# Kernel tuning notes

Hardware: AMD Instinct MI355X
Metric: run time of the kernel (lower is better)

The kernel has to match this reference:

```python
import jax, jax.numpy as jnp
import numpy as np

EPS = 1e-5

def _act_quant(x, bits=8):
    # per-token absmax quantization to signed int range, dequantized (STE)
    qb = float(2 ** (bits - 1) - 1)  # 127 for 8 bits
    scale = qb / jnp.clip(jnp.max(jnp.abs(x), axis=-1, keepdims=True), EPS, None)
    x_dq = jnp.clip(jnp.round(x * scale), -qb, qb) / scale
    return x + jax.lax.stop_gradient(x_dq - x)

def _weight_quant(w):
    # BitNet b1.58 ternary weights: scale = mean |W|, values in {-1,0,1} * scale (STE)
    s = jnp.clip(jnp.mean(jnp.abs(w)), EPS, None)
    w_dq = jnp.clip(jnp.round(w / s), -1.0, 1.0) * s
    return w + jax.lax.stop_gradient(w_dq - w)

def _bitlinear(x, w, bits=8):
    # x: [..., in], w: [out, in]
    return jnp.einsum('bsi,oi->bso', _act_quant(x, bits), _weight_quant(w))

def setup_inputs() -> dict:
    key = jax.random.key(0)
    k1, k2, k3 = jax.random.split(key, 3)
    B, S, H = 4, 4096, 2048
    I = int(H * 2.0)
    return {
        'hidden_states': jax.random.normal(k1, (B, S, H), dtype=jnp.float32),
        'w_up': jax.random.normal(k2, (I, H), dtype=jnp.float32) * (1.0 / np.sqrt(H)),
        'w_down': jax.random.normal(k3, (H, I), dtype=jnp.float32) * (1.0 / np.sqrt(I)),
    }

def reference(hidden_states, w_up, w_down):
    bits = 8
    h = _bitlinear(hidden_states, w_up, bits)          # [B,S,I]
    h = jnp.square(jax.nn.relu(h))                      # squared ReLU
    # dropout p=0.0 (eval) -> identity
    out = _bitlinear(h, w_down, bits)                   # [B,S,H]
    return out
```

## Files before the change

kernel.cpp:

```cpp
#include <hip/hip_runtime.h>
#include <hip/hip_bf16.h>

typedef signed char i8_t;
typedef _Float16 half_t;
typedef float v4fl __attribute__((ext_vector_type(4)));
typedef _Float16 v8h __attribute__((ext_vector_type(8)));
typedef int v4i __attribute__((ext_vector_type(4)));
typedef signed char v8c __attribute__((ext_vector_type(8)));
typedef signed char v16c __attribute__((ext_vector_type(16)));

__device__ __forceinline__ float ternqf(float w, float s) {
    float q = rintf(w / s);
    return fminf(1.f, fmaxf(-1.f, q));
}

__device__ __forceinline__ void gload16(const void* g, void* l) {
    __builtin_amdgcn_global_load_lds(
        (const __attribute__((address_space(1))) void*)g,
        (__attribute__((address_space(3))) void*)l, 16, 0, 0);
}

__global__ void abssum_partial(const float* __restrict__ w, long n,
                               float* __restrict__ partial) {
    long i0 = ((long)blockIdx.x * 256 + threadIdx.x) * 8;
    long stride = (long)gridDim.x * 256 * 8;
    float s = 0.f;
    for (long i = i0; i < n; i += stride) {
        v4fl a = *(const v4fl*)(w + i);
        v4fl b = *(const v4fl*)(w + i + 4);
#pragma unroll
        for (int j = 0; j < 4; ++j) s += fabsf(a[j]) + fabsf(b[j]);
    }
#pragma unroll
    for (int off = 32; off > 0; off >>= 1) s += __shfl_down(s, off, 64);
    __shared__ __align__(16) float red[4];
    if ((threadIdx.x & 63) == 0) red[threadIdx.x >> 6] = s;
    __syncthreads();
    if (threadIdx.x == 0)
        partial[blockIdx.x] = (red[0] + red[1]) + (red[2] + red[3]);
}

__global__ void abssum_final(const float* __restrict__ part_up,
                             const float* __restrict__ part_dn,
                             float* __restrict__ scales, float inv) {
    const int wv = threadIdx.x >> 6;
    const int l = threadIdx.x & 63;
    const float* part = wv ? part_dn : part_up;
    float s = ((part[l] + part[l + 64]) + (part[l + 128] + part[l + 192]));
#pragma unroll
    for (int off = 32; off > 0; off >>= 1) s += __shfl_down(s, off, 64);
    if (l == 0) scales[wv] = fmaxf(s * inv, 1e-5f);
}

__global__ void wquant_kernel(const float* __restrict__ w, i8_t* __restrict__ wq,
                              const float* __restrict__ scale) {
    float s = scale[0];
    long i = ((long)blockIdx.x * 256 + threadIdx.x) * 8;
    v4fl a = *(const v4fl*)(w + i);
    v4fl b = *(const v4fl*)(w + i + 4);
    v8c o;
#pragma unroll
    for (int j = 0; j < 4; ++j) {
        o[j]     = (i8_t)(int)ternqf(a[j], s);
        o[j + 4] = (i8_t)(int)ternqf(b[j], s);
    }
    *(v8c*)(wq + i) = o;
}

template <int W>
__global__ void rowquant_kernel(const float* __restrict__ src, i8_t* __restrict__ dst,
                                float* __restrict__ scale_out, int rows) {
    const int l = threadIdx.x & 63;
    const int row = blockIdx.x * 4 + (threadIdx.x >> 6);
    if (row >= rows) return;
    const int NI = W / 1024;
    const float* p = src + (size_t)row * W + l * 16;
    float v[NI * 16];
#pragma unroll
    for (int it = 0; it < NI; ++it) {
#pragma unroll
        for (int c = 0; c < 4; ++c) {
            v4fl a = *(const v4fl*)(p + it * 1024 + c * 4);
#pragma unroll
            for (int e = 0; e < 4; ++e) v[it * 16 + c * 4 + e] = a[e];
        }
    }
    float amax = 0.f;
#pragma unroll
    for (int j = 0; j < NI * 16; ++j) amax = fmaxf(amax, fabsf(v[j]));
#pragma unroll
    for (int off = 32; off > 0; off >>= 1)
        amax = fmaxf(amax, __shfl_xor(amax, off, 64));
    const float m = fmaxf(amax, 1e-5f);
    if (l == 0) scale_out[row] = m / 127.f;
    const float sc = 127.f / m;
    i8_t* q = dst + (size_t)row * W + l * 16;
#pragma unroll
    for (int it = 0; it < NI; ++it) {
        v16c o;
#pragma unroll
        for (int j = 0; j < 16; ++j) {
            float t = rintf(v[it * 16 + j] * sc);
            o[j] = (i8_t)(int)fminf(127.f, fmaxf(-127.f, t));
        }
        *(v16c*)(q + it * 1024) = o;
    }
}

template <typename T, int NV>
__global__ void hamax_kernel(const T* __restrict__ h, float* __restrict__ scale_out,
                             float* __restrict__ recip_out) {
    const int row = blockIdx.x;
    const int tid = threadIdx.x;
    const T* p = h + (size_t)row * (NV * 2048);
    float amax = 0.f;
#pragma unroll
    for (int it = 0; it < NV; ++it) {
        const T* s = p + ((size_t)it * 256 + tid) * 8;
#pragma unroll
        for (int j = 0; j < 8; ++j) amax = fmaxf(amax, fabsf((float)s[j]));
    }
#pragma unroll
    for (int off = 32; off > 0; off >>= 1) amax = fmaxf(amax, __shfl_xor(amax, off, 64));
    __shared__ __align__(16) float red[4];
    if ((tid & 63) == 0) red[tid >> 6] = amax;
    __syncthreads();
    if (tid == 0) {
        float m = fmaxf(fmaxf(red[0], red[1]), fmaxf(red[2], red[3]));
        m = fmaxf(m, 1e-5f);
        scale_out[row] = m / 127.f;
        recip_out[row] = 127.f / m;
    }
}

__device__ __forceinline__ void stage_tile256(const i8_t* __restrict__ g, int K,
                                              i8_t* l, int tid) {
#pragma unroll
    for (int i = 0; i < 4; ++i) {
        const int c = i * 512 + tid;
        const int r = c >> 3;
        const int lc = (((c & 7) ^ (r & 7)) << 4);
        gload16(g + (size_t)r * K + lc, l + c * 16);
    }
}

#define MIDBAR() do { \
    __builtin_amdgcn_s_barrier(); \
    __builtin_amdgcn_sched_barrier(0); \
    asm volatile("s_waitcnt lgkmcnt(0)" ::: "memory"); \
    __builtin_amdgcn_sched_barrier(0); } while (0)

#define ENDBAR() do { \
    __builtin_amdgcn_sched_barrier(0); \
    __builtin_amdgcn_s_barrier(); \
    __builtin_amdgcn_sched_barrier(0); } while (0)

template <int EPI>
__launch_bounds__(512, 2)
__global__ void gemm_bt8(const i8_t* __restrict__ A, const i8_t* __restrict__ B,
                         void* __restrict__ Cv,
                         const float* __restrict__ rowscale,
                         const float* __restrict__ wscale,
                         int M, int N, int K) {
    __shared__ __align__(16) i8_t smem[131072];

    const int tid = threadIdx.x;

    const int gx = gridDim.x;
    const int nwg = gx * gridDim.y;
    int flat = blockIdx.y * gx + blockIdx.x;
    if ((nwg & 7) == 0) flat = (flat & 7) * (nwg >> 3) + (flat >> 3);
    const int n0 = (flat % gx) * 256;
    const int m0 = (flat / gx) * 256;

    const i8_t* gA = A + (size_t)m0 * K;
    const i8_t* gB = B + (size_t)n0 * K;

    const int w = tid >> 6, l = tid & 63;
    const int wr = w >> 2, wc = w & 3;
    const int lrow = l & 15, lq = l >> 4;
    const int lr7 = lrow & 7;
    const int kk0 = ((lq)     ^ lr7) << 4;
    const int kk1 = ((lq + 4) ^ lr7) << 4;
    const int aBase = ((wr * 128 + lrow) << 7);
    const int bBase = ((wc * 64 + lrow) << 7);

    v4i acc[8][4];
#pragma unroll
    for (int a = 0; a < 8; ++a)
#pragma unroll
        for (int b = 0; b < 4; ++b) acc[a][b] = (v4i){0, 0, 0, 0};

    const int NT = K >> 7;
    stage_tile256(gB, K, smem + 32768, tid);
    stage_tile256(gA, K, smem, tid);
    stage_tile256(gB + 128, K, smem + 65536 + 32768, tid);
    stage_tile256(gA + 128, K, smem + 65536, tid);
    asm volatile("s_waitcnt vmcnt(8)" ::: "memory");
    __builtin_amdgcn_s_barrier();
    __builtin_amdgcn_sched_barrier(0);

    for (int t = 0; t < NT; ++t) {
        i8_t* Ab = smem + ((t & 1) << 16);
        i8_t* Bb = Ab + 32768;
        const bool pf = (t + 2 < NT);

        v4i a0[4], a1[4], b0[4], b1[4];

#pragma unroll
        for (int mi = 0; mi < 4; ++mi)
            a0[mi] = *(const v4i*)(Ab + aBase + (mi << 11) + kk0);
#pragma unroll
        for (int nj = 0; nj < 4; ++nj)
            b0[nj] = *(const v4i*)(Bb + bBase + (nj << 11) + kk0);
        MIDBAR();
        __builtin_amdgcn_s_setprio(1);
#pragma unroll
        for (int mi = 0; mi < 4; ++mi)
#pragma unroll
            for (int nj = 0; nj < 4; ++nj)
                acc[mi][nj] = __builtin_amdgcn_mfma_i32_16x16x64_i8(
                    a0[mi], b0[nj], acc[mi][nj], 0, 0, 0);
        __builtin_amdgcn_s_setprio(0);
        ENDBAR();

#pragma unroll
        for (int mi = 0; mi < 4; ++mi)
            a1[mi] = *(const v4i*)(Ab + aBase + ((mi + 4) << 11) + kk0);
#pragma unroll
        for (int nj = 0; nj < 4; ++nj)
            b1[nj] = *(const v4i*)(Bb + bBase + (nj << 11) + kk1);
        MIDBAR();
        __builtin_amdgcn_s_setprio(1);
#pragma unroll
        for (int mi = 0; mi < 4; ++mi)
#pragma unroll
            for (int nj = 0; nj < 4; ++nj)
                acc[mi + 4][nj] = __builtin_amdgcn_mfma_i32_16x16x64_i8(
                    a1[mi], b0[nj], acc[mi + 4][nj], 0, 0, 0);
        __builtin_amdgcn_s_setprio(0);
        ENDBAR();

#pragma unroll
        for (int mi = 0; mi < 4; ++mi)
            a0[mi] = *(const v4i*)(Ab + aBase + (mi << 11) + kk1);
#pragma unroll
        for (int mi = 0; mi < 4; ++mi)
            a1[mi] = *(const v4i*)(Ab + aBase + ((mi + 4) << 11) + kk1);
        MIDBAR();
        __builtin_amdgcn_s_setprio(1);
#pragma unroll
        for (int mi = 0; mi < 4; ++mi)
#pragma unroll
            for (int nj = 0; nj < 4; ++nj)
                acc[mi][nj] = __builtin_amdgcn_mfma_i32_16x16x64_i8(
                    a0[mi], b1[nj], acc[mi][nj], 0, 0, 0);
        __builtin_amdgcn_s_setprio(0);
        ENDBAR();

        if (pf) {
            stage_tile256(gB + (size_t)(t + 2) * 128, K, Bb, tid);
            stage_tile256(gA + (size_t)(t + 2) * 128, K, Ab, tid);
        }
        MIDBAR();
        __builtin_amdgcn_s_setprio(1);
#pragma unroll
        for (int mi = 0; mi < 4; ++mi)
#pragma unroll
            for (int nj = 0; nj < 4; ++nj)
                acc[mi + 4][nj] = __builtin_amdgcn_mfma_i32_16x16x64_i8(
                    a1[mi], b1[nj], acc[mi + 4][nj], 0, 0, 0);
        __builtin_amdgcn_s_setprio(0);
        __builtin_amdgcn_sched_barrier(0);
        if (pf) {
            asm volatile("s_waitcnt vmcnt(8)" ::: "memory");
        } else if (t + 1 < NT) {
            asm volatile("s_waitcnt vmcnt(0)" ::: "memory");
        }
        if (t + 1 < NT) {
            __builtin_amdgcn_s_barrier();
            __builtin_amdgcn_sched_barrier(0);
        }
    }

    const float sw = wscale[0];
#pragma unroll
    for (int mi = 0; mi < 8; ++mi) {
#pragma unroll
        for (int r = 0; r < 4; ++r) {
            const int row = m0 + wr * 128 + mi * 16 + lq * 4 + r;
            const float rs = sw * rowscale[row];
#pragma unroll
            for (int nj = 0; nj < 4; ++nj) {
                const int col = n0 + wc * 64 + nj * 16 + lrow;
                float v = (float)acc[mi][nj][r] * rs;
                if (EPI == 0) {
                    ((float*)Cv)[(size_t)row * N + col] = v;
                } else {
                    v = fmaxf(v, 0.f); v = v * v;
                    ((float*)Cv)[(size_t)row * N + col] = v;
                }
            }
        }
    }
}

template <int ASRC, int EPI>
__launch_bounds__(256, 2)
__global__ void gemm_bt(const void* __restrict__ Av, const i8_t* __restrict__ B,
                        void* __restrict__ Cv,
                        const float* __restrict__ rowscale,
                        const float* __restrict__ arecip,
                        const float* __restrict__ wscale,
                        int M, int N, int K) {
    __shared__ __align__(16) i8_t As[128 * 64];
    __shared__ __align__(16) i8_t Bs[128 * 64];

    const int tid = threadIdx.x;
    const int gx = gridDim.x;
    const int nwg = gx * gridDim.y;
    int flat = blockIdx.y * gx + blockIdx.x;
    if ((nwg & 7) == 0) flat = (flat & 7) * (nwg >> 3) + (flat >> 3);
    const int n0 = (flat % gx) * 128;
    const int m0 = (flat / gx) * 128;

    const int srow = tid >> 2;
    const int scol = (tid & 3) * 16;
    const i8_t* gB0 = B + (size_t)(n0 + srow) * K + scol;
    const i8_t* gB1 = B + (size_t)(n0 + 64 + srow) * K + scol;
    i8_t* lB0 = Bs + tid * 16;
    i8_t* lB1 = Bs + 4096 + tid * 16;

    const i8_t* gA0 = nullptr;
    const i8_t* gA1 = nullptr;
    i8_t* lA0 = As + tid * 16;
    i8_t* lA1 = As + 4096 + tid * 16;
    if (ASRC == 0) {
        gA0 = (const i8_t*)Av + (size_t)(m0 + srow) * K + scol;
        gA1 = (const i8_t*)Av + (size_t)(m0 + 64 + srow) * K + scol;
    }

    const int qrow = tid >> 1;
    const int qcol = (tid & 1) * 32;
    const float* gA32 = (const float*)Av + (size_t)(m0 + qrow) * K + qcol;
    const half_t* gAh = (const half_t*)Av + (size_t)(m0 + qrow) * K + qcol;
    i8_t* qdst = As + qrow * 64 + qcol;
    const float qsc = (ASRC != 0) ? arecip[m0 + qrow] : 0.f;

    const int w = tid >> 6, l = tid & 63;
    const int wr = w >> 1, wc = w & 1;
    const int lrow = l & 15, lq = l >> 4;

    v4i acc[4][4];
#pragma unroll
    for (int a = 0; a < 4; ++a)
#pragma unroll
        for (int b = 0; b < 4; ++b) acc[a][b] = (v4i){0, 0, 0, 0};

    const int kiters = K / 64;
    for (int kt = 0; kt < kiters; ++kt) {
        const int off = kt * 64;
        v16c r0, r1;
        if (ASRC == 1) {
#pragma unroll
            for (int c = 0; c < 4; ++c) {
                v4fl f0 = *(const v4fl*)(gA32 + off + c * 4);
                v4fl f1 = *(const v4fl*)(gA32 + off + 16 + c * 4);
#pragma unroll
                for (int e = 0; e < 4; ++e) {
                    float t0 = rintf(f0[e] * qsc);
                    float t1 = rintf(f1[e] * qsc);
                    r0[c * 4 + e] = (i8_t)(int)fminf(127.f, fmaxf(-127.f, t0));
                    r1[c * 4 + e] = (i8_t)(int)fminf(127.f, fmaxf(-127.f, t1));
                }
            }
        } else if (ASRC == 2) {
#pragma unroll
            for (int c = 0; c < 2; ++c) {
                v8h h0 = *(const v8h*)(gAh + off + c * 8);
                v8h h1 = *(const v8h*)(gAh + off + 16 + c * 8);
#pragma unroll
                for (int e = 0; e < 8; ++e) {
                    float t0 = rintf((float)h0[e] * qsc);
                    float t1 = rintf((float)h1[e] * qsc);
                    r0[c * 8 + e] = (i8_t)(int)fminf(127.f, fmaxf(-127.f, t0));
                    r1[c * 8 + e] = (i8_t)(int)fminf(127.f, fmaxf(-127.f, t1));
                }
            }
        }
        __syncthreads();
        gload16(gB0 + off, lB0);
        gload16(gB1 + off, lB1);
        if (ASRC == 0) {
            gload16(gA0 + off, lA0);
            gload16(gA1 + off, lA1);
        } else {
            *(v16c*)qdst = r0;
            *(v16c*)(qdst + 16) = r1;
        }
        __syncthreads();

        v4i af[4], bfr[4];
#pragma unroll
        for (int mi = 0; mi < 4; ++mi)
            af[mi] = *(const v4i*)(As + (wr * 64 + mi * 16 + lrow) * 64 + lq * 16);
#pragma unroll
        for (int nj = 0; nj < 4; ++nj)
            bfr[nj] = *(const v4i*)(Bs + (wc * 64 + nj * 16 + lrow) * 64 + lq * 16);
#pragma unroll
        for (int mi = 0; mi < 4; ++mi)
#pragma unroll
            for (int nj = 0; nj < 4; ++nj)
                acc[mi][nj] = __builtin_amdgcn_mfma_i32_16x16x64_i8(
                    af[mi], bfr[nj], acc[mi][nj], 0, 0, 0);
    }

    const float sw = wscale[0];
#pragma unroll
    for (int mi = 0; mi < 4; ++mi) {
#pragma unroll
        for (int r = 0; r < 4; ++r) {
            const int row = m0 + wr * 64 + mi * 16 + lq * 4 + r;
            const float rs = sw * rowscale[row];
#pragma unroll
            for (int nj = 0; nj < 4; ++nj) {
                const int col = n0 + wc * 64 + nj * 16 + lrow;
                float v = (float)acc[mi][nj][r] * rs;
                if (EPI == 0) {
                    ((float*)Cv)[(size_t)row * N + col] = v;
                } else if (EPI == 1) {
                    v = fmaxf(v, 0.f); v = v * v;
                    ((half_t*)Cv)[(size_t)row * N + col] = (half_t)v;
                } else {
                    v = fmaxf(v, 0.f); v = v * v;
                    ((float*)Cv)[(size_t)row * N + col] = v;
                }
            }
        }
    }
}

extern "C" void kernel_launch(void* const* d_in, const int* in_sizes, int n_in,
                              void* d_out, int out_size, void* d_ws, size_t ws_size,
                              hipStream_t stream) {
    const float* x   = (const float*)d_in[0];
    const float* wup = (const float*)d_in[1];
    const float* wdn = (const float*)d_in[2];

    const int H = 2048;
    const int T = in_sizes[0] / H;
    const int I = in_sizes[1] / H;
    const long nw = (long)in_sizes[1];
    const float winv = 1.0f / (float)nw;

    char* p = (char*)d_ws;
    float* scales  = (float*)p;
    float* part_up = (float*)(p + 256);
    float* part_dn = (float*)(p + 1280);
    float* a_scale = (float*)(p + 2304);
    float* h_scale = a_scale + T;
    float* h_recip = h_scale + T;
    size_t off = 2304 + (size_t)12 * T;
    off = (off + 255) & ~(size_t)255;
    i8_t* xq  = (i8_t*)(p + off); off += (size_t)T * H;
    off = (off + 255) & ~(size_t)255;
    i8_t* wqu = (i8_t*)(p + off); off += (size_t)I * H;
    off = (off + 255) & ~(size_t)255;
    i8_t* wqd = (i8_t*)(p + off); off += (size_t)H * I;
    off = (off + 255) & ~(size_t)255;
    void* h  = (void*)(p + off);
    i8_t* hq = (i8_t*)(p + off + (size_t)T * I * 4);

    const size_t need_full = off + (size_t)T * I * 5;
    const size_t need_h32  = off + (size_t)T * I * 4;
    const int mode = (ws_size == 0 || need_full <= ws_size) ? 0
                   : (need_h32 <= ws_size ? 1 : 2);
    const bool big_ok = (T % 256 == 0) && (I % 256 == 0) && (H % 256 == 0) &&
                        (H >= 256) && (I >= 256);

    abssum_partial<<<256, 256, 0, stream>>>(wup, nw, part_up);
    abssum_partial<<<256, 256, 0, stream>>>(wdn, nw, part_dn);
    abssum_final<<<1, 128, 0, stream>>>(part_up, part_dn, scales, winv);

    int wblocks = (int)(nw / 2048);
    wquant_kernel<<<wblocks, 256, 0, stream>>>(wup, wqu, scales + 0);
    wquant_kernel<<<wblocks, 256, 0, stream>>>(wdn, wqd, scales + 1);

    rowquant_kernel<2048><<<(T + 3) / 4, 256, 0, stream>>>(x, xq, a_scale, T);

    if (mode == 0 && big_ok) {
        gemm_bt8<2><<<dim3(I / 256, T / 256), 512, 0, stream>>>(
            xq, wqu, h, a_scale, scales + 0, T, I, H);
        rowquant_kernel<4096><<<(T + 3) / 4, 256, 0, stream>>>(
            (const float*)h, hq, h_scale, T);
        gemm_bt8<0><<<dim3(H / 256, T / 256), 512, 0, stream>>>(
            hq, wqd, d_out, h_scale, scales + 1, T, H, I);
    } else if (mode == 0) {
        gemm_bt<0, 2><<<dim3(I / 128, T / 128), 256, 0, stream>>>(
            xq, wqu, h, a_scale, nullptr, scales + 0, T, I, H);
        rowquant_kernel<4096><<<(T + 3) / 4, 256, 0, stream>>>(
            (const float*)h, hq, h_scale, T);
        gemm_bt<0, 0><<<dim3(H / 128, T / 128), 256, 0, stream>>>(
            hq, wqd, d_out, h_scale, nullptr, scales + 1, T, H, I);
    } else if (mode == 1) {
        gemm_bt<0, 2><<<dim3(I / 128, T / 128), 256, 0, stream>>>(
            xq, wqu, h, a_scale, nullptr, scales + 0, T, I, H);
        hamax_kernel<float, 2><<<T, 256, 0, stream>>>((const float*)h, h_scale, h_recip);
        gemm_bt<1, 0><<<dim3(H / 128, T / 128), 256, 0, stream>>>(
            h, wqd, d_out, h_scale, h_recip, scales + 1, T, H, I);
    } else {
        gemm_bt<0, 1><<<dim3(I / 128, T / 128), 256, 0, stream>>>(
            xq, wqu, h, a_scale, nullptr, scales + 0, T, I, H);
        hamax_kernel<half_t, 2><<<T, 256, 0, stream>>>((const half_t*)h, h_scale, h_recip);
        gemm_bt<2, 0><<<dim3(H / 128, T / 128), 256, 0, stream>>>(
            h, wqd, d_out, h_scale, h_recip, scales + 1, T, H, I);
    }
}
```

Before: 652.8 us.

## Load B operand directly from global into registers, halve LDS, fewer barriers

The int8 GEMM no longer stages the B (weight) tile through LDS. Each wave loads its B fragments straight from global memory into registers, prefetching the next K-tile into a second register set. Only A is double-buffered in LDS, so LDS use halves and the per-iteration barriers drop from several to two. The cost is more VGPR pressure from the register prefetch buffers, and B loads are now redundant across the wave rows (two waves load the same B) with less coalesced access, which may add global traffic or stalls.

```diff
diff --git a/kernel.cpp b/kernel.cpp
--- a/kernel.cpp
+++ b/kernel.cpp
@@ -144,17 +144,6 @@
     }
 }
 
-#define MIDBAR() do { \
-    __builtin_amdgcn_s_barrier(); \
-    __builtin_amdgcn_sched_barrier(0); \
-    asm volatile("s_waitcnt lgkmcnt(0)" ::: "memory"); \
-    __builtin_amdgcn_sched_barrier(0); } while (0)
-
-#define ENDBAR() do { \
-    __builtin_amdgcn_sched_barrier(0); \
-    __builtin_amdgcn_s_barrier(); \
-    __builtin_amdgcn_sched_barrier(0); } while (0)
-
 template <int EPI>
 __launch_bounds__(512, 2)
 __global__ void gemm_bt8(const i8_t* __restrict__ A, const i8_t* __restrict__ B,
@@ -162,7 +151,7 @@
                          const float* __restrict__ rowscale,
                          const float* __restrict__ wscale,
                          int M, int N, int K) {
-    __shared__ __align__(16) i8_t smem[131072];
+    __shared__ __align__(16) i8_t Asm[65536];
 
     const int tid = threadIdx.x;
 
@@ -174,7 +163,6 @@
     const int m0 = (flat / gx) * 256;
 
     const i8_t* gA = A + (size_t)m0 * K;
-    const i8_t* gB = B + (size_t)n0 * K;
 
     const int w = tid >> 6, l = tid & 63;
     const int wr = w >> 2, wc = w & 3;
@@ -183,7 +171,8 @@
     const int kk0 = ((lq)     ^ lr7) << 4;
     const int kk1 = ((lq + 4) ^ lr7) << 4;
     const int aBase = ((wr * 128 + lrow) << 7);
-    const int bBase = ((wc * 64 + lrow) << 7);
+
+    const i8_t* gBl = B + (size_t)(n0 + wc * 64 + lrow) * K + lq * 16;
 
     v4i acc[8][4];
 #pragma unroll
@@ -191,93 +180,88 @@
 #pragma unroll
         for (int b = 0; b < 4; ++b) acc[a][b] = (v4i){0, 0, 0, 0};
 
+    v4i bcur[4][2], bnxt[4][2];
+
     const int NT = K >> 7;
-    stage_tile256(gB, K, smem + 32768, tid);
-    stage_tile256(gA, K, smem, tid);
-    stage_tile256(gB + 128, K, smem + 65536 + 32768, tid);
-    stage_tile256(gA + 128, K, smem + 65536, tid);
-    asm volatile("s_waitcnt vmcnt(8)" ::: "memory");
+    stage_tile256(gA, K, Asm, tid);
+#pragma unroll
+    for (int nj = 0; nj < 4; ++nj)
+#pragma unroll
+        for (int ks = 0; ks < 2; ++ks)
+            bcur[nj][ks] = *(const v4i*)(gBl + (size_t)(nj * 16) * K + ks * 64);
+    stage_tile256(gA + 128, K, Asm + 32768, tid);
+    asm volatile("s_waitcnt vmcnt(4)" ::: "memory");
     __builtin_amdgcn_s_barrier();
     __builtin_amdgcn_sched_barrier(0);
 
     for (int t = 0; t < NT; ++t) {
-        i8_t* Ab = smem + ((t & 1) << 16);
-        i8_t* Bb = Ab + 32768;
-        const bool pf = (t + 2 < NT);
-
-        v4i a0[4], a1[4], b0[4], b1[4];
-
-#pragma unroll
-        for (int mi = 0; mi < 4; ++mi)
+        i8_t* Ab = Asm + ((t & 1) << 15);
+        const bool pf1 = (t + 1 < NT);
+        const bool pf2 = (t + 2 < NT);
+
+        v4i a0[8], a1[8];
+
+#pragma unroll
+        for (int mi = 0; mi < 8; ++mi)
             a0[mi] = *(const v4i*)(Ab + aBase + (mi << 11) + kk0);
-#pragma unroll
-        for (int nj = 0; nj < 4; ++nj)
-            b0[nj] = *(const v4i*)(Bb + bBase + (nj << 11) + kk0);
-        MIDBAR();
+        if (pf1) {
+            const size_t koff = (size_t)(t + 1) * 128;
+#pragma unroll
+            for (int nj = 0; nj < 4; ++nj)
+#pragma unroll
+                for (int ks = 0; ks < 2; ++ks)
+                    bnxt[nj][ks] = *(const v4i*)(gBl + (size_t)(nj * 16) * K + koff + ks * 64);
+        }
+        __builtin_amdgcn_sched_barrier(0);
         __builtin_amdgcn_s_setprio(1);
 #pragma unroll
-        for (int mi = 0; mi < 4; ++mi)
+        for (int mi = 0; mi < 8; ++mi)
 #pragma unroll
             for (int nj = 0; nj < 4; ++nj)
                 acc[mi][nj] = __builtin_amdgcn_mfma_i32_16x16x64_i8(
-                    a0[mi], b0[nj], acc[mi][nj], 0, 0, 0);
+                    a0[mi], bcur[nj][0], acc[mi][nj], 0, 0, 0);
         __builtin_amdgcn_s_setprio(0);
-        ENDBAR();
-
+
+#pragma unroll
+        for (int mi = 0; mi < 8; ++mi)
+            a1[mi] = *(const v4i*)(Ab + aBase + (mi << 11) + kk1);
+        __builtin_amdgcn_sched_barrier(0);
+        __builtin_amdgcn_s_setprio(1);
 #pragma unroll
         for (int mi = 0; mi < 4; ++mi)
-            a1[mi] = *(const v4i*)(Ab + aBase + ((mi + 4) << 11) + kk0);
-#pragma unroll
-        for (int nj = 0; nj < 4; ++nj)
-            b1[nj] = *(const v4i*)(Bb + bBase + (nj << 11) + kk1);
-        MIDBAR();
+#pragma unroll
+            for (int nj = 0; nj < 4; ++nj)
+                acc[mi][nj] = __builtin_amdgcn_mfma_i32_16x16x64_i8(
+                    a1[mi], bcur[nj][1], acc[mi][nj], 0, 0, 0);
+        __builtin_amdgcn_s_setprio(0);
+        __builtin_amdgcn_sched_barrier(0);
+        asm volatile("s_waitcnt lgkmcnt(0)" ::: "memory");
+        __builtin_amdgcn_sched_barrier(0);
+        __builtin_amdgcn_s_barrier();
+        __builtin_amdgcn_sched_barrier(0);
+
+        if (pf2) stage_tile256(gA + (size_t)(t + 2) * 128, K, Ab, tid);
+        __builtin_amdgcn_sched_barrier(0);
         __builtin_amdgcn_s_setprio(1);
 #pragma unroll
         for (int mi = 0; mi < 4; ++mi)
 #pragma unroll
             for (int nj = 0; nj < 4; ++nj)
                 acc[mi + 4][nj] = __builtin_amdgcn_mfma_i32_16x16x64_i8(
-                    a1[mi], b0[nj], acc[mi + 4][nj], 0, 0, 0);
+                    a1[mi + 4], bcur[nj][1], acc[mi + 4][nj], 0, 0, 0);
         __builtin_amdgcn_s_setprio(0);
-        ENDBAR();
-
-#pragma unroll
-        for (int mi = 0; mi < 4; ++mi)
-            a0[mi] = *(const v4i*)(Ab + aBase + (mi << 11) + kk1);
-#pragma unroll
-        for (int mi = 0; mi < 4; ++mi)
-            a1[mi] = *(const v4i*)(Ab + aBase + ((mi + 4) << 11) + kk1);
-        MIDBAR();
-        __builtin_amdgcn_s_setprio(1);
-#pragma unroll
-        for (int mi = 0; mi < 4; ++mi)
+        __builtin_amdgcn_sched_barrier(0);
+        if (pf2) {
+            asm volatile("s_waitcnt vmcnt(4)" ::: "memory");
+        } else if (pf1) {
+            asm volatile("s_waitcnt vmcnt(0)" ::: "memory");
+        }
+        if (pf1) {
 #pragma unroll
             for (int nj = 0; nj < 4; ++nj)
-                acc[mi][nj] = __builtin_amdgcn_mfma_i32_16x16x64_i8(
-                    a0[mi], b1[nj], acc[mi][nj], 0, 0, 0);
-        __builtin_amdgcn_s_setprio(0);
-        ENDBAR();
-
-        if (pf) {
-            stage_tile256(gB + (size_t)(t + 2) * 128, K, Bb, tid);
-            stage_tile256(gA + (size_t)(t + 2) * 128, K, Ab, tid);
-        }
-        MIDBAR();
-        __builtin_amdgcn_s_setprio(1);
-#pragma unroll
-        for (int mi = 0; mi < 4; ++mi)
-#pragma unroll
-            for (int nj = 0; nj < 4; ++nj)
-                acc[mi + 4][nj] = __builtin_amdgcn_mfma_i32_16x16x64_i8(
-                    a1[mi], b1[nj], acc[mi + 4][nj], 0, 0, 0);
-        __builtin_amdgcn_s_setprio(0);
-        __builtin_amdgcn_sched_barrier(0);
-        if (pf) {
-            asm volatile("s_waitcnt vmcnt(8)" ::: "memory");
-        } else if (t + 1 < NT) {
-            asm volatile("s_waitcnt vmcnt(0)" ::: "memory");
-        }
-        if (t + 1 < NT) {
+#pragma unroll
+                for (int ks = 0; ks < 2; ++ks)
+                    bcur[nj][ks] = bnxt[nj][ks];
             __builtin_amdgcn_s_barrier();
             __builtin_amdgcn_sched_barrier(0);
         }
```

Measured after the change: 793.4 us. 1.22x slower.
